# Performance work log

Hardware: AMD Instinct MI355X
Metric: run time of the kernel (lower is better)

The kernel has to match this reference:

```python
import jax, jax.numpy as jnp
import numpy as np

B, H, W = 16, 512, 512
N_BINS = 511          # round(mean(shape)) - 1 for (512, 512)
MAX_R = 1.0           # (1 + min(shape)/max(shape)) / 2 for square image


def _bin_ids():
    # Precompute per-pixel radial shell index (replaces the list of boolean shell masks).
    frame = max(H, W)
    xx, yy = np.mgrid[:H, :W]
    ellipse = ((xx - H / 2) * 2 / frame) ** 2 + ((yy - W / 2) * 2 / frame) ** 2
    r2 = np.linspace(0.0, MAX_R, N_BINS + 1)[1:] ** 2
    # shell k = { r2[k-1] <= ellipse < r2[k] }; pixels with ellipse >= r2[-1] map to
    # overflow bin N_BINS and are dropped, exactly matching the xor'd ellipse masks.
    return jnp.asarray(np.searchsorted(r2, ellipse.ravel(), side='right').astype(np.int32))


BIN_IDS = _bin_ids()  # [H*W] int32 in [0, N_BINS]


def setup_inputs() -> dict:
    key = jax.random.key(0)
    k1, k2 = jax.random.split(key)
    return {
        "z_": jax.random.normal(k1, (B, H, W, 2), dtype=jnp.float32),
        "t_": jax.random.normal(k2, (B, H, W, 2), dtype=jnp.float32),
    }


def _shell_sums(x):
    # x: [B, H*W] -> per-shell sums [B, N_BINS+1] in a single fused segment-sum pass.
    return jax.vmap(lambda v: jax.ops.segment_sum(v, BIN_IDS, num_segments=N_BINS + 1))(x)


def reference(z_, t_):
    tc = t_[..., 0] + 1j * t_[..., 1]          # [B,H,W] complex target
    zc = z_[..., 0] + 1j * z_[..., 1]
    Ft = jnp.fft.fft2(tc, axes=(-2, -1))
    Fe = jnp.fft.fft2(zc - tc, axes=(-2, -1))
    norm_coeff = Ft.real ** 2 + Ft.imag ** 2   # |FFT(target)|^2, [B,H,W]
    errors = Fe.real ** 2 + Fe.imag ** 2       # |FFT(z - target)|^2
    es = _shell_sums(errors.reshape(B, -1))[:, :N_BINS]      # drop overflow bin
    ns = _shell_sums(norm_coeff.reshape(B, -1))[:, :N_BINS]
    nre = es / jnp.maximum(ns, 1e-8)           # per-batch, per-shell normed error
    # per_shell_loss = per-batch sum over shells; loss = mean over batch
    return jnp.mean(jnp.sum(nre, axis=1))
```

## Files before the change

### kernel.cpp

```cpp
#include <hip/hip_runtime.h>

#define HH 512
#define WW 512
#define NBATCH 16
#define NBINS 512

#define PI_F 3.14159265358979323846f

#define SW(r) ((r) ^ (((r) >> 4) & 0xF))
#define TSW(c, hh) (((c) << 3) + ((hh) ^ (((c) >> 1) & 7)))

__device__ __forceinline__ float2 cadd(float2 a, float2 b){ return make_float2(a.x+b.x, a.y+b.y); }
__device__ __forceinline__ float2 csub(float2 a, float2 b){ return make_float2(a.x-b.x, a.y-b.y); }
__device__ __forceinline__ float2 cmul(float2 a, float2 b){
    return make_float2(a.x*b.x - a.y*b.y, a.x*b.y + a.y*b.x);
}

__device__ __forceinline__ void dft8(const float2* a, float2* y) {
    const float s2 = 0.70710678118654752440f;
    float2 t02a = cadd(a[0], a[4]), t02s = csub(a[0], a[4]);
    float2 t13a = cadd(a[2], a[6]), t13s = csub(a[2], a[6]);
    float2 E0 = cadd(t02a, t13a);
    float2 E2 = csub(t02a, t13a);
    float2 E1 = make_float2(t02s.x + t13s.y, t02s.y - t13s.x);
    float2 E3 = make_float2(t02s.x - t13s.y, t02s.y + t13s.x);
    float2 u02a = cadd(a[1], a[5]), u02s = csub(a[1], a[5]);
    float2 u13a = cadd(a[3], a[7]), u13s = csub(a[3], a[7]);
    float2 O0 = cadd(u02a, u13a);
    float2 O2 = csub(u02a, u13a);
    float2 O1 = make_float2(u02s.x + u13s.y, u02s.y - u13s.x);
    float2 O3 = make_float2(u02s.x - u13s.y, u02s.y + u13s.x);
    float2 wO1 = make_float2(s2 * (O1.x + O1.y), s2 * (O1.y - O1.x));
    float2 wO2 = make_float2(O2.y, -O2.x);
    float2 wO3 = make_float2(s2 * (O3.y - O3.x), -s2 * (O3.x + O3.y));
    y[0] = cadd(E0, O0);  y[4] = csub(E0, O0);
    y[1] = cadd(E1, wO1); y[5] = csub(E1, wO1);
    y[2] = cadd(E2, wO2); y[6] = csub(E2, wO2);
    y[3] = cadd(E3, wO3); y[7] = csub(E3, wO3);
}

__device__ __forceinline__ void twiddle8(float base, float2* w) {
    float s1, c1, s4, c4;
    __sincosf(base, &s1, &c1);
    __sincosf(4.0f * base, &s4, &c4);
    w[0] = make_float2(1.0f, 0.0f);
    w[1] = make_float2(c1, s1);
    w[2] = cmul(w[1], w[1]);
    w[3] = cmul(w[2], w[1]);
    w[4] = make_float2(c4, s4);
    w[5] = cmul(w[4], w[1]);
    w[6] = cmul(w[4], w[2]);
    w[7] = cmul(w[4], w[3]);
}

__device__ __forceinline__ void fft512_stage0_store(float2* rb, int lane, const float2* a) {
    float2 y[8]; dft8(a, y);
    float2 w[8]; twiddle8(-PI_F * (float)lane * (1.0f / 256.0f), w);
#pragma unroll
    for (int r = 0; r < 8; ++r) rb[SW(8 * lane + r)] = cmul(y[r], w[r]);
}

__device__ __forceinline__ void fft512_stage1(float2* rb, int lane) {
    float2 a[8];
#pragma unroll
    for (int u = 0; u < 8; ++u) a[u] = rb[SW(lane + 64 * u)];
    float2 y[8]; dft8(a, y);
    float2 w[8]; twiddle8(-PI_F * (float)(lane >> 3) * (1.0f / 32.0f), w);
    const int qb = (lane & 7) + ((lane >> 3) << 6);
#pragma unroll
    for (int r = 0; r < 8; ++r) rb[SW(qb + 8 * r)] = cmul(y[r], w[r]);
}

__device__ __forceinline__ void fft512_stage2(const float2* rb, int lane, float2* y) {
    float2 a[8];
#pragma unroll
    for (int u = 0; u < 8; ++u) a[u] = rb[SW(lane + 64 * u)];
    dft8(a, y);
}

__global__ __launch_bounds__(512, 4)
void row_fft_kernel(const float2* __restrict__ z, const float2* __restrict__ t,
                    float2* __restrict__ fieldsT, int b0) {
    __shared__ float2 buf[8 * 512];
    const int tid  = threadIdx.x;
    const int lane = tid & 63;
    const int g    = tid >> 6;
    const int bid  = blockIdx.x;
    const int hg   = bid & 63;
    const int lb   = bid >> 6;
    const int b    = b0 + lb;
    const int h    = (hg << 3) | g;
    const size_t rowOff = ((size_t)(b * HH + h)) * WW;

    const float2* tr = t + rowOff;
    const float2* zr = z + rowOff;
    float2 tv[8], zv[8];
#pragma unroll
    for (int u = 0; u < 8; ++u) tv[u] = tr[lane + 64 * u];
#pragma unroll
    for (int u = 0; u < 8; ++u) zv[u] = zr[lane + 64 * u];

    float2* rb = buf + (g << 9);
#pragma unroll
    for (int f = 0; f < 2; ++f) {
        float2 a[8];
        if (f == 0) {
#pragma unroll
            for (int u = 0; u < 8; ++u) a[u] = tv[u];
        } else {
#pragma unroll
            for (int u = 0; u < 8; ++u) a[u] = make_float2(zv[u].x - tv[u].x,
                                                           zv[u].y - tv[u].y);
        }
        fft512_stage0_store(rb, lane, a);
        __builtin_amdgcn_wave_barrier();
        fft512_stage1(rb, lane);
        __builtin_amdgcn_wave_barrier();
        float2 y[8];
        fft512_stage2(rb, lane, y);

        __syncthreads();
#pragma unroll
        for (int r = 0; r < 8; ++r) {
            int c = lane + (r << 6);
            buf[TSW(c, g)] = y[r];
        }
        __syncthreads();
        float2* outF = fieldsT + ((size_t)(lb * 2 + f) << 18);
#pragma unroll
        for (int k = 0; k < 8; ++k) {
            int e  = tid + (k << 9);
            int c  = e >> 3;
            int hh = e & 7;
            outF[((size_t)c << 9) + (hg << 3) + hh] = buf[TSW(c, hh)];
        }
        __syncthreads();
    }
}

__global__ __launch_bounds__(512, 4)
void col_fft_bin_kernel(const float2* __restrict__ fieldsT,
                        float* __restrict__ bins, int b0) {
    __shared__ float2 buf[8 * 512];
    __shared__ float hist[NBINS];
    const int tid  = threadIdx.x;
    const int lane = tid & 63;
    const int g    = tid >> 6;
    const int bid  = blockIdx.x;
    const int cg   = bid & 63;
    const int fl   = bid >> 6;
    const int f    = fl & 1;
    const int b    = b0 + (fl >> 1);
    const int c    = (cg << 3) | g;

    hist[tid] = 0.0f;
    __syncthreads();

    const float2* colT = fieldsT + (((size_t)fl << 9) + c) * 512;
    float2 a[8];
#pragma unroll
    for (int u = 0; u < 8; ++u) a[u] = colT[lane + (u << 6)];

    float2* rb = buf + (g << 9);
    fft512_stage0_store(rb, lane, a);
    __builtin_amdgcn_wave_barrier();
    fft512_stage1(rb, lane);
    __builtin_amdgcn_wave_barrier();
    float2 y[8];
    fft512_stage2(rb, lane, y);

    const float fcv = (float)(c - 256) * (1.0f / 256.0f);
    const float fc2 = fcv * fcv;
#pragma unroll
    for (int r = 0; r < 8; ++r) {
        int k = lane + (r << 6);
        float fr = (float)(k - 256) * (1.0f / 256.0f);
        float e = fr * fr + fc2;
        if (e < 1.0f) {
            int bin = (int)(sqrt((double)e) * 511.0);
            atomicAdd(&hist[bin], y[r].x * y[r].x + y[r].y * y[r].y);
        }
    }
    __syncthreads();
    atomicAdd(&bins[((size_t)f * NBATCH + b) * NBINS + tid], hist[tid]);
}

__global__ __launch_bounds__(512)
void loss_kernel(const float* __restrict__ bins, float* __restrict__ outp) {
    __shared__ float red[512];
    const int tid = threadIdx.x;
    float acc = 0.0f;
    if (tid < 511) {
#pragma unroll 4
        for (int b = 0; b < NBATCH; ++b) {
            float ns = bins[((size_t)b) * NBINS + tid];
            float es = bins[((size_t)(NBATCH + b)) * NBINS + tid];
            acc += es / fmaxf(ns, 1e-8f);
        }
    }
    red[tid] = acc;
    __syncthreads();
    for (int s = 256; s > 0; s >>= 1) {
        if (tid < s) red[tid] += red[tid + s];
        __syncthreads();
    }
    if (tid == 0) outp[0] = red[0] * (1.0f / NBATCH);
}

extern "C" void kernel_launch(void* const* d_in, const int* in_sizes, int n_in,
                              void* d_out, int out_size, void* d_ws, size_t ws_size,
                              hipStream_t stream) {
    const float2* z = (const float2*)d_in[0];
    const float2* t = (const float2*)d_in[1];
    float* outp = (float*)d_out;

    const size_t binsBytes = (size_t)2 * NBATCH * NBINS * sizeof(float);
    const size_t fpb = (size_t)2 * HH * WW * sizeof(float2);

    int CB = 16;
    while (CB > 1 && binsBytes + (size_t)CB * fpb > ws_size) CB >>= 1;

    float*  bins    = (float*)d_ws;
    float2* fieldsT = (float2*)((char*)d_ws + binsBytes);

    hipMemsetAsync(bins, 0, binsBytes, stream);

    for (int b0 = 0; b0 < NBATCH; b0 += CB) {
        row_fft_kernel<<<CB * 64, 512, 0, stream>>>(z, t, fieldsT, b0);
        col_fft_bin_kernel<<<CB * 2 * 64, 512, 0, stream>>>(fieldsT, bins, b0);
    }
    loss_kernel<<<1, 512, 0, stream>>>(bins, outp);
}
```

Baseline: 158.2 us.

## Store intermediate row FFT in fp16 and process two FFTs per wave

Intermediate transposed row-FFT output is packed to half precision (cvt_pkrtz), halving the bytes written and re-read between the row and column kernels. Each wave now computes two 512-point FFTs interleaved, sharing twiddles and raising ILP. The row kernel handles 16 rows per block and writes uint4 vectors, the column kernel uses 256-thread blocks, and the chunked batching loop is removed, so the whole intermediate buffer is assumed to fit in the workspace. The bin index now uses float sqrt instead of double. The fp16 intermediate introduces rounding and range risk for the FFT values, which could hurt accuracy.

```diff
diff --git a/kernel.cpp b/kernel.cpp
--- a/kernel.cpp
+++ b/kernel.cpp
@@ -8,12 +8,22 @@
 #define PI_F 3.14159265358979323846f
 
 #define SW(r) ((r) ^ (((r) >> 4) & 0xF))
-#define TSW(c, hh) (((c) << 3) + ((hh) ^ (((c) >> 1) & 7)))
 
 __device__ __forceinline__ float2 cadd(float2 a, float2 b){ return make_float2(a.x+b.x, a.y+b.y); }
 __device__ __forceinline__ float2 csub(float2 a, float2 b){ return make_float2(a.x-b.x, a.y-b.y); }
 __device__ __forceinline__ float2 cmul(float2 a, float2 b){
     return make_float2(a.x*b.x - a.y*b.y, a.x*b.y + a.y*b.x);
+}
+
+typedef __fp16 h2v __attribute__((ext_vector_type(2)));
+__device__ __forceinline__ unsigned pack2(float2 v) {
+    union { h2v h; unsigned u; } c;
+    c.h = __builtin_amdgcn_cvt_pkrtz(v.x, v.y);
+    return c.u;
+}
+__device__ __forceinline__ float2 unpack2(unsigned u) {
+    union { unsigned u; __fp16 h[2]; } c; c.u = u;
+    return make_float2((float)c.h[0], (float)c.h[1]);
 }
 
 __device__ __forceinline__ void dft8(const float2* a, float2* y) {
@@ -53,94 +63,111 @@
     w[7] = cmul(w[4], w[3]);
 }
 
-__device__ __forceinline__ void fft512_stage0_store(float2* rb, int lane, const float2* a) {
-    float2 y[8]; dft8(a, y);
-    float2 w[8]; twiddle8(-PI_F * (float)lane * (1.0f / 256.0f), w);
-#pragma unroll
-    for (int r = 0; r < 8; ++r) rb[SW(8 * lane + r)] = cmul(y[r], w[r]);
-}
-
-__device__ __forceinline__ void fft512_stage1(float2* rb, int lane) {
-    float2 a[8];
-#pragma unroll
-    for (int u = 0; u < 8; ++u) a[u] = rb[SW(lane + 64 * u)];
-    float2 y[8]; dft8(a, y);
-    float2 w[8]; twiddle8(-PI_F * (float)(lane >> 3) * (1.0f / 32.0f), w);
+__device__ __forceinline__ void fft512_x2(float2* rb0, float2* rb1, int lane,
+                                          float2* a0, float2* a1,
+                                          float2* y0, float2* y1) {
+    float2 w[8], y[8];
+    twiddle8(-PI_F * (float)lane * (1.0f / 256.0f), w);
+    dft8(a0, y);
+#pragma unroll
+    for (int r = 0; r < 8; ++r) rb0[SW(8 * lane + r)] = cmul(y[r], w[r]);
+    dft8(a1, y);
+#pragma unroll
+    for (int r = 0; r < 8; ++r) rb1[SW(8 * lane + r)] = cmul(y[r], w[r]);
+    __builtin_amdgcn_wave_barrier();
+#pragma unroll
+    for (int u = 0; u < 8; ++u) a0[u] = rb0[SW(lane + 64 * u)];
+#pragma unroll
+    for (int u = 0; u < 8; ++u) a1[u] = rb1[SW(lane + 64 * u)];
+    twiddle8(-PI_F * (float)(lane >> 3) * (1.0f / 32.0f), w);
     const int qb = (lane & 7) + ((lane >> 3) << 6);
-#pragma unroll
-    for (int r = 0; r < 8; ++r) rb[SW(qb + 8 * r)] = cmul(y[r], w[r]);
-}
-
-__device__ __forceinline__ void fft512_stage2(const float2* rb, int lane, float2* y) {
-    float2 a[8];
-#pragma unroll
-    for (int u = 0; u < 8; ++u) a[u] = rb[SW(lane + 64 * u)];
-    dft8(a, y);
+    dft8(a0, y);
+#pragma unroll
+    for (int r = 0; r < 8; ++r) rb0[SW(qb + 8 * r)] = cmul(y[r], w[r]);
+    dft8(a1, y);
+#pragma unroll
+    for (int r = 0; r < 8; ++r) rb1[SW(qb + 8 * r)] = cmul(y[r], w[r]);
+    __builtin_amdgcn_wave_barrier();
+#pragma unroll
+    for (int u = 0; u < 8; ++u) a0[u] = rb0[SW(lane + 64 * u)];
+#pragma unroll
+    for (int u = 0; u < 8; ++u) a1[u] = rb1[SW(lane + 64 * u)];
+    dft8(a0, y0);
+    dft8(a1, y1);
 }
 
 __global__ __launch_bounds__(512, 4)
 void row_fft_kernel(const float2* __restrict__ z, const float2* __restrict__ t,
-                    float2* __restrict__ fieldsT, int b0) {
-    __shared__ float2 buf[8 * 512];
+                    unsigned* __restrict__ fieldsT) {
+    __shared__ float2 buf[16 * 512];
     const int tid  = threadIdx.x;
     const int lane = tid & 63;
     const int g    = tid >> 6;
     const int bid  = blockIdx.x;
-    const int hg   = bid & 63;
-    const int lb   = bid >> 6;
-    const int b    = b0 + lb;
-    const int h    = (hg << 3) | g;
-    const size_t rowOff = ((size_t)(b * HH + h)) * WW;
-
-    const float2* tr = t + rowOff;
-    const float2* zr = z + rowOff;
-    float2 tv[8], zv[8];
-#pragma unroll
-    for (int u = 0; u < 8; ++u) tv[u] = tr[lane + 64 * u];
-#pragma unroll
-    for (int u = 0; u < 8; ++u) zv[u] = zr[lane + 64 * u];
-
-    float2* rb = buf + (g << 9);
+    const int hg   = bid & 31;
+    const int b    = bid >> 5;
+    const int hb   = hg << 4;
+    const int r0   = hb | (g << 1);
+    const size_t off0 = (((size_t)b * HH) + r0) << 9;
+    const size_t off1 = off0 + 512;
+
+    float2* rb0 = buf + ((g << 1) << 9);
+    float2* rb1 = rb0 + 512;
+    unsigned* tile = (unsigned*)buf;
+
 #pragma unroll
     for (int f = 0; f < 2; ++f) {
-        float2 a[8];
+        float2 a0[8], a1[8];
         if (f == 0) {
 #pragma unroll
-            for (int u = 0; u < 8; ++u) a[u] = tv[u];
+            for (int u = 0; u < 8; ++u) a0[u] = t[off0 + lane + 64 * u];
+#pragma unroll
+            for (int u = 0; u < 8; ++u) a1[u] = t[off1 + lane + 64 * u];
         } else {
 #pragma unroll
-            for (int u = 0; u < 8; ++u) a[u] = make_float2(zv[u].x - tv[u].x,
-                                                           zv[u].y - tv[u].y);
-        }
-        fft512_stage0_store(rb, lane, a);
-        __builtin_amdgcn_wave_barrier();
-        fft512_stage1(rb, lane);
-        __builtin_amdgcn_wave_barrier();
-        float2 y[8];
-        fft512_stage2(rb, lane, y);
-
-        __syncthreads();
+            for (int u = 0; u < 8; ++u) {
+                float2 zv = z[off0 + lane + 64 * u];
+                float2 tv = t[off0 + lane + 64 * u];
+                a0[u] = make_float2(zv.x - tv.x, zv.y - tv.y);
+            }
+#pragma unroll
+            for (int u = 0; u < 8; ++u) {
+                float2 zv = z[off1 + lane + 64 * u];
+                float2 tv = t[off1 + lane + 64 * u];
+                a1[u] = make_float2(zv.x - tv.x, zv.y - tv.y);
+            }
+        }
+        float2 y0[8], y1[8];
+        fft512_x2(rb0, rb1, lane, a0, a1, y0, y1);
+
+        __syncthreads();
+        const int rr0 = g << 1, rr1 = rr0 | 1;
 #pragma unroll
         for (int r = 0; r < 8; ++r) {
             int c = lane + (r << 6);
-            buf[TSW(c, g)] = y[r];
-        }
-        __syncthreads();
-        float2* outF = fieldsT + ((size_t)(lb * 2 + f) << 18);
-#pragma unroll
-        for (int k = 0; k < 8; ++k) {
-            int e  = tid + (k << 9);
-            int c  = e >> 3;
-            int hh = e & 7;
-            outF[((size_t)c << 9) + (hg << 3) + hh] = buf[TSW(c, hh)];
-        }
-        __syncthreads();
-    }
-}
-
-__global__ __launch_bounds__(512, 4)
-void col_fft_bin_kernel(const float2* __restrict__ fieldsT,
-                        float* __restrict__ bins, int b0) {
+            tile[rr0 * 516 + c] = pack2(y0[r]);
+            tile[rr1 * 516 + c] = pack2(y1[r]);
+        }
+        __syncthreads();
+        unsigned* outF = fieldsT + (((size_t)(b * 2 + f)) << 18);
+#pragma unroll
+        for (int k = 0; k < 4; ++k) {
+            int e = tid + (k << 9);
+            int c = e >> 2, q = e & 3;
+            uint4 v;
+            v.x = tile[(4 * q + 0) * 516 + c];
+            v.y = tile[(4 * q + 1) * 516 + c];
+            v.z = tile[(4 * q + 2) * 516 + c];
+            v.w = tile[(4 * q + 3) * 516 + c];
+            *(uint4*)(outF + (((size_t)c) << 9) + hb + (q << 2)) = v;
+        }
+        __syncthreads();
+    }
+}
+
+__global__ __launch_bounds__(256, 4)
+void col_fft_bin_kernel(const unsigned* __restrict__ fieldsT,
+                        float* __restrict__ bins) {
     __shared__ float2 buf[8 * 512];
     __shared__ float hist[NBINS];
     const int tid  = threadIdx.x;
@@ -150,39 +177,49 @@
     const int cg   = bid & 63;
     const int fl   = bid >> 6;
     const int f    = fl & 1;
-    const int b    = b0 + (fl >> 1);
-    const int c    = (cg << 3) | g;
+    const int b    = fl >> 1;
+    const int cA   = (cg << 3) | (g << 1);
 
     hist[tid] = 0.0f;
+    hist[tid + 256] = 0.0f;
     __syncthreads();
 
-    const float2* colT = fieldsT + (((size_t)fl << 9) + c) * 512;
-    float2 a[8];
-#pragma unroll
-    for (int u = 0; u < 8; ++u) a[u] = colT[lane + (u << 6)];
-
-    float2* rb = buf + (g << 9);
-    fft512_stage0_store(rb, lane, a);
-    __builtin_amdgcn_wave_barrier();
-    fft512_stage1(rb, lane);
-    __builtin_amdgcn_wave_barrier();
-    float2 y[8];
-    fft512_stage2(rb, lane, y);
-
-    const float fcv = (float)(c - 256) * (1.0f / 256.0f);
-    const float fc2 = fcv * fcv;
+    const unsigned* colA = fieldsT + ((((size_t)fl) << 9) + cA) * 512;
+    const unsigned* colB = colA + 512;
+    float2 a0[8], a1[8];
+#pragma unroll
+    for (int u = 0; u < 8; ++u) a0[u] = unpack2(colA[lane + (u << 6)]);
+#pragma unroll
+    for (int u = 0; u < 8; ++u) a1[u] = unpack2(colB[lane + (u << 6)]);
+
+    float2* rb0 = buf + ((g << 1) << 9);
+    float2* rb1 = rb0 + 512;
+    float2 y0[8], y1[8];
+    fft512_x2(rb0, rb1, lane, a0, a1, y0, y1);
+
+    const float fcA = (float)(cA - 256)     * (1.0f / 256.0f);
+    const float fcB = (float)(cA + 1 - 256) * (1.0f / 256.0f);
+    const float fc2A = fcA * fcA, fc2B = fcB * fcB;
 #pragma unroll
     for (int r = 0; r < 8; ++r) {
         int k = lane + (r << 6);
         float fr = (float)(k - 256) * (1.0f / 256.0f);
-        float e = fr * fr + fc2;
-        if (e < 1.0f) {
-            int bin = (int)(sqrt((double)e) * 511.0);
-            atomicAdd(&hist[bin], y[r].x * y[r].x + y[r].y * y[r].y);
+        float fr2 = fr * fr;
+        float eA = fr2 + fc2A;
+        float eB = fr2 + fc2B;
+        if (eA < 1.0f) {
+            int bin = (int)(sqrtf(eA) * 511.0f);
+            atomicAdd(&hist[bin], y0[r].x * y0[r].x + y0[r].y * y0[r].y);
+        }
+        if (eB < 1.0f) {
+            int bin = (int)(sqrtf(eB) * 511.0f);
+            atomicAdd(&hist[bin], y1[r].x * y1[r].x + y1[r].y * y1[r].y);
         }
     }
     __syncthreads();
-    atomicAdd(&bins[((size_t)f * NBATCH + b) * NBINS + tid], hist[tid]);
+    float* gb = bins + ((size_t)f * NBATCH + b) * NBINS;
+    atomicAdd(&gb[tid],       hist[tid]);
+    atomicAdd(&gb[tid + 256], hist[tid + 256]);
 }
 
 __global__ __launch_bounds__(512)
@@ -215,19 +252,12 @@
     float* outp = (float*)d_out;
 
     const size_t binsBytes = (size_t)2 * NBATCH * NBINS * sizeof(float);
-    const size_t fpb = (size_t)2 * HH * WW * sizeof(float2);
-
-    int CB = 16;
-    while (CB > 1 && binsBytes + (size_t)CB * fpb > ws_size) CB >>= 1;
-
-    float*  bins    = (float*)d_ws;
-    float2* fieldsT = (float2*)((char*)d_ws + binsBytes);
-
-    hipMemsetAsync(bins, 0, binsBytes, stream);
-
-    for (int b0 = 0; b0 < NBATCH; b0 += CB) {
-        row_fft_kernel<<<CB * 64, 512, 0, stream>>>(z, t, fieldsT, b0);
-        col_fft_bin_kernel<<<CB * 2 * 64, 512, 0, stream>>>(fieldsT, bins, b0);
-    }
+    float*    bins    = (float*)d_ws;
+    unsigned* fieldsT = (unsigned*)((char*)d_ws + binsBytes);
+
+    (void)hipMemsetAsync(bins, 0, binsBytes, stream);
+
+    row_fft_kernel<<<NBATCH * 32, 512, 0, stream>>>(z, t, fieldsT);
+    col_fft_bin_kernel<<<NBATCH * 2 * 64, 256, 0, stream>>>(fieldsT, bins);
     loss_kernel<<<1, 512, 0, stream>>>(bins, outp);
 }
```

Result: slower. 173.6 us (+9.8%).
